# Performance work log

Hardware: AMD Instinct MI355X
Metric: run time of the kernel (lower is better)

Reference implementation:

```python
import jax, jax.numpy as jnp
import numpy as np

NUM_NODES = 100000
EMB = 16
LAT = 8
EDGE_DIM = 32
E = 1600000


def setup_inputs() -> dict:
    key = jax.random.key(0)
    ks = jax.random.split(key, 12)
    s = 0.05
    return {
        "edge_index": jax.random.randint(ks[0], (2, E), 0, NUM_NODES),
        "edge_attr": jax.random.normal(ks[1], (E, EDGE_DIM), dtype=jnp.float32),
        "node_emb": jax.random.normal(ks[2], (NUM_NODES, EMB), dtype=jnp.float32) * s,
        "ew_W1": jax.random.normal(ks[3], (EDGE_DIM, 64), dtype=jnp.float32) * s,
        "ew_b1": jnp.zeros((64,), jnp.float32),
        "ew_W2": jax.random.normal(ks[4], (64, EMB * LAT), dtype=jnp.float32) * s,
        "ew_b2": jnp.zeros((EMB * LAT,), jnp.float32),
        "root_W": jax.random.normal(ks[5], (EMB, LAT), dtype=jnp.float32) * s,
        "conv_b": jnp.zeros((LAT,), jnp.float32),
        "dec_W1": jax.random.normal(ks[6], (2 * LAT, 64), dtype=jnp.float32) * s,
        "dec_b1": jnp.zeros((64,), jnp.float32),
        "dec_W2": jax.random.normal(ks[7], (64, EDGE_DIM), dtype=jnp.float32) * s,
        "dec_b2": jnp.zeros((EDGE_DIM,), jnp.float32),
    }


def reference(edge_index, edge_attr, node_emb, ew_W1, ew_b1, ew_W2, ew_b2,
              root_W, conv_b, dec_W1, dec_b1, dec_W2, dec_b2):
    src, tgt = edge_index[0], edge_index[1]
    # edge MLP -> per-edge weight matrix (E, EMB, LAT)
    h = jax.nn.relu(edge_attr @ ew_W1 + ew_b1)
    theta = (h @ ew_W2 + ew_b2).reshape(-1, EMB, LAT)
    # per-edge matmul on gathered source features
    msg = jnp.einsum('ei,eio->eo', node_emb[src], theta)  # (E, LAT)
    # scatter-mean to targets
    agg = jax.ops.segment_sum(msg, tgt, num_segments=NUM_NODES)
    cnt = jax.ops.segment_sum(jnp.ones((msg.shape[0],), msg.dtype), tgt, num_segments=NUM_NODES)
    agg = agg / jnp.maximum(cnt, 1.0)[:, None]
    # NNConv root weight + bias
    latent = node_emb @ root_W + agg + conv_b  # (N, LAT)
    # decode: gather-concat-MLP on edges
    edge_in = jnp.concatenate([latent[src], latent[tgt]], axis=1)  # (E, 2*LAT)
    out = jax.nn.relu(edge_in @ dec_W1 + dec_b1) @ dec_W2 + dec_b2  # (E, EDGE_DIM)
    return out
```

## Files before the change

kernel.cpp:

```cpp
#include <hip/hip_runtime.h>
#include <hip/hip_bf16.h>

typedef __attribute__((ext_vector_type(8))) short  s16x8;
typedef __attribute__((ext_vector_type(4))) float  f32x4;

constexpr int EMB  = 16;
constexpr int LAT  = 8;
constexpr int EDIM = 32;
constexpr int HID  = 64;

constexpr int BSHIFT = 7;
constexpr int BNODES = 1 << BSHIFT;
constexpr int PCHUNK = 8192;

__device__ __forceinline__ short f2b(float f) {
  __hip_bfloat16 h = __float2bfloat16(f);
  return __builtin_bit_cast(short, h);
}
__device__ __forceinline__ float asf(unsigned int u) { return __builtin_bit_cast(float, u); }
__device__ __forceinline__ unsigned int pk2(float lo, float hi) {
  return ((unsigned int)(unsigned short)f2b(hi) << 16) |
         (unsigned int)(unsigned short)f2b(lo);
}

#define FIXSCALE 1.0995116277760e12f
#define FIXINV   9.094947017729282e-13

__global__ void prep_kernel(const float* __restrict__ W1, const float* __restrict__ W2,
                            const float* __restrict__ b2,
                            const float* __restrict__ dW1, const float* __restrict__ dW2,
                            short* __restrict__ W1c, short* __restrict__ W2p,
                            unsigned int* __restrict__ b2pp,
                            short* __restrict__ dW1c, short* __restrict__ dW2p) {
  int t = blockIdx.x * blockDim.x + threadIdx.x;
  if (t < 64 * 32) { int c = t / 32, k = t % 32; W1c[t] = f2b(W1[k * 64 + c]); }
  if (t < 8192) {
    int ct2 = t >> 10, kt = (t >> 9) & 1, lh = (t >> 7) & 3, r = (t >> 3) & 15, j = t & 7;
    int k = (kt * 2 + (j >> 2)) * 16 + lh * 4 + (j & 3);
    int i = 2 * ct2 + ((r >> 1) & 1);
    int o = 2 * (r >> 2) + (r & 1);
    W2p[t] = f2b(W2[k * 128 + i * 8 + o]);
  }
  if (t < 64) {
    int lh = t >> 4, slot = t & 15;
    int ct2 = slot >> 1, ih = slot & 1;
    int i = 2 * ct2 + ih;
    unsigned int lo = (unsigned short)f2b(b2[i * 8 + 2 * lh]);
    unsigned int hi = (unsigned short)f2b(b2[i * 8 + 2 * lh + 1]);
    b2pp[t] = (hi << 16) | lo;
  }
  if (t < 64 * 16) { int c = t / 16, k = t % 16; dW1c[t] = f2b(dW1[k * 64 + c]); }
  if (t < 2048) {
    int ct2 = t >> 10, kt = (t >> 9) & 1, lh = (t >> 7) & 3, r = (t >> 3) & 15, j = t & 7;
    int k = (kt * 2 + (j >> 2)) * 16 + lh * 4 + (j & 3);
    dW2p[t] = f2b(dW2[k * 32 + ct2 * 16 + r]);
  }
}

__global__ __launch_bounds__(256) void bhist_kernel(const int* __restrict__ ei,
                                                    int* __restrict__ bins,
                                                    int E, int nbuck) {
  __shared__ int h[1024];
  for (int i = threadIdx.x; i < nbuck; i += 256) h[i] = 0;
  __syncthreads();
  for (int e = blockIdx.x * blockDim.x + threadIdx.x; e < E; e += gridDim.x * blockDim.x)
    atomicAdd(&h[ei[E + e] >> BSHIFT], 1);
  __syncthreads();
  for (int i = threadIdx.x; i < nbuck; i += 256)
    if (h[i]) atomicAdd(&bins[i], h[i]);
}

__global__ __launch_bounds__(1024) void bscan_kernel(const int* __restrict__ bins,
                                                     int* __restrict__ bases,
                                                     int* __restrict__ cursor, int nbuck) {
  __shared__ int sh[1024];
  int tid = threadIdx.x;
  int v = (tid < nbuck) ? bins[tid] : 0;
  sh[tid] = v;
  __syncthreads();
  for (int off = 1; off < 1024; off <<= 1) {
    int t = (tid >= off) ? sh[tid - off] : 0;
    __syncthreads();
    sh[tid] += t;
    __syncthreads();
  }
  int ex = sh[tid] - v;
  if (tid < nbuck) { bases[tid] = ex; cursor[tid] = ex; }
  if (tid == 0) bases[nbuck] = sh[1023];
}

__global__ __launch_bounds__(256) void part_kernel(const int* __restrict__ ei,
                                                   int* __restrict__ cursor,
                                                   unsigned int* __restrict__ recs,
                                                   int E, int nbuck) {
  __shared__ int h[1024];
  __shared__ int gcl[1024];
  __shared__ int lr[1024];
  const int tid  = threadIdx.x;
  const int base = blockIdx.x * PCHUNK;

  for (int i = tid; i < nbuck; i += 256) { h[i] = 0; lr[i] = 0; }
  __syncthreads();
  for (int i = tid; i < PCHUNK; i += 256) {
    int e = base + i;
    if (e < E) atomicAdd(&h[ei[E + e] >> BSHIFT], 1);
  }
  __syncthreads();
  for (int i = tid; i < nbuck; i += 256)
    gcl[i] = h[i] ? atomicAdd(&cursor[i], h[i]) : 0;
  __syncthreads();
  for (int i = tid; i < PCHUNK; i += 256) {
    int e = base + i;
    if (e >= E) continue;
    int tgt = ei[E + e];
    int b = tgt >> BSHIFT;
    int p = gcl[b] + atomicAdd(&lr[b], 1);
    recs[p] = ((unsigned int)e << BSHIFT) | (unsigned int)(tgt & (BNODES - 1));
  }
}

__global__ __launch_bounds__(256, 2) void encagg_kernel(
    const int* __restrict__ ei, const float* __restrict__ attr,
    const float* __restrict__ emb,
    const short* __restrict__ W1c, const float* __restrict__ b1,
    const short* __restrict__ W2p, const unsigned int* __restrict__ b2pp,
    const unsigned int* __restrict__ recs, const int* __restrict__ bases,
    const float* __restrict__ rootW, const float* __restrict__ convb,
    float* __restrict__ latent, int N, int E) {
  __shared__ short lds_w1[2048];
  __shared__ short lds_w2[8192];
  __shared__ float lds_b1[64];
  __shared__ unsigned int lds_b2[64];
  __shared__ long long acc[BNODES][LAT];
  __shared__ int cnt[BNODES];
  __shared__ float rw[EMB * LAT];
  __shared__ float cb[LAT];

  const int tid = threadIdx.x;
  const int w = tid >> 6, l = tid & 63;
  const int lh = l >> 4, ll = l & 15;
  const int b = blockIdx.x;

  {
    reinterpret_cast<int4*>(lds_w1)[tid] = reinterpret_cast<const int4*>(W1c)[tid];
#pragma unroll
    for (int i = 0; i < 4; i++)
      reinterpret_cast<int4*>(lds_w2)[i * 256 + tid] =
          reinterpret_cast<const int4*>(W2p)[i * 256 + tid];
    if (tid < 64) lds_b1[tid] = b1[tid];
    if (tid < 64) lds_b2[tid] = b2pp[tid];
    long long* af0 = &acc[0][0];
    for (int i = tid; i < BNODES * LAT; i += 256) af0[i] = 0;
    if (tid < BNODES) cnt[tid] = 0;
    if (tid < EMB * LAT) rw[tid] = rootW[tid];
    if (tid < LAT) cb[tid] = convb[tid];
  }
  __syncthreads();

  const int s = bases[b], epos = bases[b + 1];
  const int nrec = epos - s;
  const f32x4 z = {0.f, 0.f, 0.f, 0.f};

  for (int g = w * 64; g < nrec; g += 256) {
    const int base = s + g;
    int ridx = min(base + l, epos - 1);
    unsigned int rec = recs[ridx];
    int eid = (int)(rec >> BSHIFT);
    int tl  = (int)(rec & (BNODES - 1));
    unsigned int xqp[8];
    {
      int src = ei[eid];
      const float4* er = reinterpret_cast<const float4*>(emb) + (size_t)src * 4;
      float4 v0 = er[0], v1 = er[1], v2 = er[2], v3 = er[3];
      xqp[0] = pk2(v0.x, v0.y); xqp[1] = pk2(v0.z, v0.w);
      xqp[2] = pk2(v1.x, v1.y); xqp[3] = pk2(v1.z, v1.w);
      xqp[4] = pk2(v2.x, v2.y); xqp[5] = pk2(v2.z, v2.w);
      xqp[6] = pk2(v3.x, v3.y); xqp[7] = pk2(v3.z, v3.w);
    }
    s16x8 afs[4];
#pragma unroll
    for (int mt = 0; mt < 4; mt++) {
      int rowE = __shfl(eid, mt * 16 + ll, 64);
      const float4* ap = reinterpret_cast<const float4*>(attr + (size_t)rowE * EDIM + lh * 8);
      float4 a0 = ap[0], a1 = ap[1];
      afs[mt][0]=f2b(a0.x); afs[mt][1]=f2b(a0.y); afs[mt][2]=f2b(a0.z); afs[mt][3]=f2b(a0.w);
      afs[mt][4]=f2b(a1.x); afs[mt][5]=f2b(a1.y); afs[mt][6]=f2b(a1.z); afs[mt][7]=f2b(a1.w);
    }

#pragma unroll
    for (int mt = 0; mt < 4; mt++) {
      f32x4 c1t[4];
#pragma unroll
      for (int ct = 0; ct < 4; ct++) {
        s16x8 b1f = *reinterpret_cast<const s16x8*>(lds_w1 + (ct * 16 + ll) * 32 + lh * 8);
        c1t[ct] = __builtin_amdgcn_mfma_f32_16x16x32_bf16(b1f, afs[mt], z, 0, 0, 0);
      }
      short hb[4][4];
#pragma unroll
      for (int ct = 0; ct < 4; ct++) {
        float4 bv = *reinterpret_cast<const float4*>(lds_b1 + ct * 16 + lh * 4);
        hb[ct][0] = f2b(fmaxf(c1t[ct][0] + bv.x, 0.f));
        hb[ct][1] = f2b(fmaxf(c1t[ct][1] + bv.y, 0.f));
        hb[ct][2] = f2b(fmaxf(c1t[ct][2] + bv.z, 0.f));
        hb[ct][3] = f2b(fmaxf(c1t[ct][3] + bv.w, 0.f));
      }
      s16x8 a2f0, a2f1;
#pragma unroll
      for (int j = 0; j < 8; j++) a2f0[j] = hb[(j >> 2)][j & 3];
#pragma unroll
      for (int j = 0; j < 8; j++) a2f1[j] = hb[2 + (j >> 2)][j & 3];

      const int srcl = mt * 16 + ll;
      unsigned int xs[8];
#pragma unroll
      for (int c = 0; c < 8; c++)
        xs[c] = (unsigned int)__shfl((int)xqp[c], srcl, 64);
      int tlv = __shfl(tl, srcl, 64);

      float q0 = 0.f, q1 = 0.f;
#pragma unroll
      for (int ct2 = 0; ct2 < 8; ct2++) {
        s16x8 f0 = *reinterpret_cast<const s16x8*>(lds_w2 + ((ct2 * 2 + 0) * 4 + lh) * 128 + ll * 8);
        s16x8 f1 = *reinterpret_cast<const s16x8*>(lds_w2 + ((ct2 * 2 + 1) * 4 + lh) * 128 + ll * 8);
        f32x4 c2 = __builtin_amdgcn_mfma_f32_16x16x32_bf16(f0, a2f0, z, 0, 0, 0);
        c2 = __builtin_amdgcn_mfma_f32_16x16x32_bf16(f1, a2f1, c2, 0, 0, 0);
        uint2 pp = *reinterpret_cast<const uint2*>(lds_b2 + lh * 16 + 2 * ct2);
        float b00 = asf(pp.x << 16), b01 = asf(pp.x & 0xffff0000u);
        float b10 = asf(pp.y << 16), b11 = asf(pp.y & 0xffff0000u);
        float xv0 = asf(xs[ct2] << 16);
        float xv1 = asf(xs[ct2] & 0xffff0000u);
        q0 = fmaf(xv0, c2[0] + b00, q0);
        q1 = fmaf(xv0, c2[1] + b01, q1);
        q0 = fmaf(xv1, c2[2] + b10, q0);
        q1 = fmaf(xv1, c2[3] + b11, q1);
      }
      if (base + srcl < epos) {
        atomicAdd((unsigned long long*)&acc[tlv][2 * lh],
                  (unsigned long long)(long long)(q0 * FIXSCALE));
        atomicAdd((unsigned long long*)&acc[tlv][2 * lh + 1],
                  (unsigned long long)(long long)(q1 * FIXSCALE));
        if (lh == 0) atomicAdd(&cnt[tlv], 1);
      }
    }
  }
  __syncthreads();

  int n = b * BNODES + tid;
  if (tid < BNODES && n < N) {
    float inv = 1.f / fmaxf((float)cnt[tid], 1.f);
    float r[LAT];
#pragma unroll
    for (int o = 0; o < LAT; o++)
      r[o] = fmaf((float)((double)acc[tid][o] * FIXINV), inv, cb[o]);

    float x[EMB];
    const float4* np4 = reinterpret_cast<const float4*>(emb) + (size_t)n * (EMB / 4);
#pragma unroll
    for (int i = 0; i < EMB / 4; i++) {
      float4 v = np4[i];
      x[4 * i + 0] = v.x; x[4 * i + 1] = v.y; x[4 * i + 2] = v.z; x[4 * i + 3] = v.w;
    }
#pragma unroll
    for (int i = 0; i < EMB; i++)
#pragma unroll
      for (int o = 0; o < LAT; o++) r[o] = fmaf(x[i], rw[i * LAT + o], r[o]);

    float4* lp = reinterpret_cast<float4*>(latent) + (size_t)n * 2;
    lp[0] = make_float4(r[0], r[1], r[2], r[3]);
    lp[1] = make_float4(r[4], r[5], r[6], r[7]);
  }
}

__global__ __launch_bounds__(256, 4) void dec_mfma_kernel(
    const int* __restrict__ ei, const float* __restrict__ lat,
    const short* __restrict__ dW1c, const float* __restrict__ db1,
    const short* __restrict__ dW2p, const float* __restrict__ db2,
    float* __restrict__ out, int E) {
  __shared__ short lds_w1[2048];
  __shared__ short lds_w2[2048];
  __shared__ float lds_b1[64];
  __shared__ float lds_b2[32];

  const int tid = threadIdx.x;
  const int w = tid >> 6, l = tid & 63;
  const int lh = l >> 4, ll = l & 15;
  const int ebase = blockIdx.x * 256 + w * 64;

  {
    if (tid < 128) {
      int4 v = reinterpret_cast<const int4*>(dW1c)[tid];
      int hid = tid >> 1, kb = (tid & 1) * 8;
      *reinterpret_cast<int4*>(lds_w1 + hid * 32 + kb) = v;
      *reinterpret_cast<int4*>(lds_w1 + hid * 32 + 16 + kb) = make_int4(0, 0, 0, 0);
    }
    reinterpret_cast<int4*>(lds_w2)[tid] = reinterpret_cast<const int4*>(dW2p)[tid];
    if (tid < 64) lds_b1[tid] = db1[tid];
    if (tid < 32) lds_b2[tid] = db2[tid];
  }
  __syncthreads();

  const f32x4 z = {0.f, 0.f, 0.f, 0.f};

#pragma unroll
  for (int mt = 0; mt < 4; mt++) {
    s16x8 af = (s16x8){0, 0, 0, 0, 0, 0, 0, 0};
    if (lh < 2) {
      int rowA = min(ebase + mt * 16 + ll, E - 1);
      int node = ei[(lh == 0 ? 0 : E) + rowA];
      const float4* lp = reinterpret_cast<const float4*>(lat + (size_t)node * LAT);
      float4 p0 = lp[0], p1 = lp[1];
      af[0]=f2b(p0.x); af[1]=f2b(p0.y); af[2]=f2b(p0.z); af[3]=f2b(p0.w);
      af[4]=f2b(p1.x); af[5]=f2b(p1.y); af[6]=f2b(p1.z); af[7]=f2b(p1.w);
    }

    f32x4 c1t[4];
#pragma unroll
    for (int ct = 0; ct < 4; ct++) {
      s16x8 b1f = *reinterpret_cast<const s16x8*>(lds_w1 + (ct * 16 + ll) * 32 + lh * 8);
      c1t[ct] = __builtin_amdgcn_mfma_f32_16x16x32_bf16(b1f, af, z, 0, 0, 0);
    }

    short hb[4][4];
#pragma unroll
    for (int ct = 0; ct < 4; ct++) {
      float4 bv = *reinterpret_cast<const float4*>(lds_b1 + ct * 16 + lh * 4);
      hb[ct][0] = f2b(fmaxf(c1t[ct][0] + bv.x, 0.f));
      hb[ct][1] = f2b(fmaxf(c1t[ct][1] + bv.y, 0.f));
      hb[ct][2] = f2b(fmaxf(c1t[ct][2] + bv.z, 0.f));
      hb[ct][3] = f2b(fmaxf(c1t[ct][3] + bv.w, 0.f));
    }
    s16x8 a2f0, a2f1;
#pragma unroll
    for (int j = 0; j < 8; j++) a2f0[j] = hb[(j >> 2)][j & 3];
#pragma unroll
    for (int j = 0; j < 8; j++) a2f1[j] = hb[2 + (j >> 2)][j & 3];

    int e = ebase + mt * 16 + ll;
#pragma unroll
    for (int ct2 = 0; ct2 < 2; ct2++) {
      s16x8 f0 = *reinterpret_cast<const s16x8*>(lds_w2 + ((ct2 * 2 + 0) * 4 + lh) * 128 + ll * 8);
      s16x8 f1 = *reinterpret_cast<const s16x8*>(lds_w2 + ((ct2 * 2 + 1) * 4 + lh) * 128 + ll * 8);
      f32x4 c2 = __builtin_amdgcn_mfma_f32_16x16x32_bf16(f0, a2f0, z, 0, 0, 0);
      c2 = __builtin_amdgcn_mfma_f32_16x16x32_bf16(f1, a2f1, c2, 0, 0, 0);
      float4 bv = *reinterpret_cast<const float4*>(lds_b2 + ct2 * 16 + lh * 4);
      if (e < E)
        *reinterpret_cast<float4*>(out + (size_t)e * EDIM + ct2 * 16 + lh * 4) =
            make_float4(c2[0] + bv.x, c2[1] + bv.y, c2[2] + bv.z, c2[3] + bv.w);
    }
  }
}

extern "C" void kernel_launch(void* const* d_in, const int* in_sizes, int n_in,
                              void* d_out, int out_size, void* d_ws, size_t ws_size,
                              hipStream_t stream) {
  const int*   ei    = (const int*)  d_in[0];
  const float* attr  = (const float*)d_in[1];
  const float* emb   = (const float*)d_in[2];
  const float* ewW1  = (const float*)d_in[3];
  const float* ewb1  = (const float*)d_in[4];
  const float* ewW2  = (const float*)d_in[5];
  const float* ewb2  = (const float*)d_in[6];
  const float* rootW = (const float*)d_in[7];
  const float* convb = (const float*)d_in[8];
  const float* dW1   = (const float*)d_in[9];
  const float* db1   = (const float*)d_in[10];
  const float* dW2   = (const float*)d_in[11];
  const float* db2   = (const float*)d_in[12];
  float* out = (float*)d_out;

  const int E     = in_sizes[0] / 2;
  const int N     = in_sizes[2] / EMB;
  const int nbuck = (N + BNODES - 1) >> BSHIFT;

  short* W1c  = (short*)d_ws;
  short* W2p  = W1c + 64 * 32;
  short* dW1c = W2p + 8192;
  short* dW2p = dW1c + 64 * 16;
  unsigned int* b2pp = (unsigned int*)(dW2p + 2048);
  float* lat  = (float*)(b2pp + 64);
  unsigned int* recs = (unsigned int*)(lat + (size_t)N * LAT);
  int* bins   = (int*)(recs + E);
  int* bases  = bins + nbuck;
  int* cursor = bases + nbuck + 1;

  const int blocks_e = (E + 255) / 256;
  const int blocks_p = (E + PCHUNK - 1) / PCHUNK;

  hipMemsetAsync(bins, 0, (size_t)nbuck * sizeof(int), stream);
  prep_kernel<<<32, 256, 0, stream>>>(ewW1, ewW2, ewb2, dW1, dW2,
                                      W1c, W2p, b2pp, dW1c, dW2p);
  bhist_kernel<<<256, 256, 0, stream>>>(ei, bins, E, nbuck);
  bscan_kernel<<<1, 1024, 0, stream>>>(bins, bases, cursor, nbuck);
  part_kernel<<<blocks_p, 256, 0, stream>>>(ei, cursor, recs, E, nbuck);
  encagg_kernel<<<nbuck, 256, 0, stream>>>(ei, attr, emb, W1c, ewb1, W2p, b2pp,
                                           recs, bases, rootW, convb, lat, N, E);
  dec_mfma_kernel<<<blocks_e, 256, 0, stream>>>(ei, lat, dW1c, db1, dW2p, db2, out, E);
}
```

Baseline: 223.2 us.

## Halve node buckets, pre-swizzle MFMA weight fragments, pad accumulator, raise occupancy

Node buckets shrink from 128 to 64 nodes, which doubles the number of encode/aggregate blocks, and the scan now handles two bins per thread to cover up to 2048 buckets. First-layer weights for the encoder and decoder are pre-swizzled into a fragment-contiguous layout so each lane's LDS read is contiguous, replacing the strided reads. The shared int64 accumulator gets a padding column to cut bank conflicts, and the encoder launch bound moves to 4 blocks per CU. In exchange, each block does less work relative to its fixed cost of loading weights into LDS, and the extra blocks and higher occupancy put more pressure on registers.

```diff
diff --git a/kernel.cpp b/kernel.cpp
--- a/kernel.cpp
+++ b/kernel.cpp
@@ -9,9 +9,10 @@
 constexpr int EDIM = 32;
 constexpr int HID  = 64;
 
-constexpr int BSHIFT = 7;
+constexpr int BSHIFT = 6;
 constexpr int BNODES = 1 << BSHIFT;
 constexpr int PCHUNK = 8192;
+constexpr int MAXBUCK = 2048;
 
 __device__ __forceinline__ short f2b(float f) {
   __hip_bfloat16 h = __float2bfloat16(f);
@@ -29,11 +30,14 @@
 __global__ void prep_kernel(const float* __restrict__ W1, const float* __restrict__ W2,
                             const float* __restrict__ b2,
                             const float* __restrict__ dW1, const float* __restrict__ dW2,
-                            short* __restrict__ W1c, short* __restrict__ W2p,
+                            short* __restrict__ W1f, short* __restrict__ W2p,
                             unsigned int* __restrict__ b2pp,
-                            short* __restrict__ dW1c, short* __restrict__ dW2p) {
+                            short* __restrict__ dW1f, short* __restrict__ dW2p) {
   int t = blockIdx.x * blockDim.x + threadIdx.x;
-  if (t < 64 * 32) { int c = t / 32, k = t % 32; W1c[t] = f2b(W1[k * 64 + c]); }
+  if (t < 2048) {
+    int j = t & 7, ll = (t >> 3) & 15, lh = (t >> 7) & 3, ct = t >> 9;
+    W1f[t] = f2b(W1[(lh * 8 + j) * 64 + ct * 16 + ll]);
+  }
   if (t < 8192) {
     int ct2 = t >> 10, kt = (t >> 9) & 1, lh = (t >> 7) & 3, r = (t >> 3) & 15, j = t & 7;
     int k = (kt * 2 + (j >> 2)) * 16 + lh * 4 + (j & 3);
@@ -49,7 +53,10 @@
     unsigned int hi = (unsigned short)f2b(b2[i * 8 + 2 * lh + 1]);
     b2pp[t] = (hi << 16) | lo;
   }
-  if (t < 64 * 16) { int c = t / 16, k = t % 16; dW1c[t] = f2b(dW1[k * 64 + c]); }
+  if (t < 4096) {
+    int j = t & 7, ll = (t >> 3) & 15, lh = (t >> 7) & 3, ct = t >> 9;
+    dW1f[t] = (lh < 2) ? f2b(dW1[(lh * 8 + j) * 64 + ct * 16 + ll]) : (short)0;
+  }
   if (t < 2048) {
     int ct2 = t >> 10, kt = (t >> 9) & 1, lh = (t >> 7) & 3, r = (t >> 3) & 15, j = t & 7;
     int k = (kt * 2 + (j >> 2)) * 16 + lh * 4 + (j & 3);
@@ -60,7 +67,7 @@
 __global__ __launch_bounds__(256) void bhist_kernel(const int* __restrict__ ei,
                                                     int* __restrict__ bins,
                                                     int E, int nbuck) {
-  __shared__ int h[1024];
+  __shared__ int h[MAXBUCK];
   for (int i = threadIdx.x; i < nbuck; i += 256) h[i] = 0;
   __syncthreads();
   for (int e = blockIdx.x * blockDim.x + threadIdx.x; e < E; e += gridDim.x * blockDim.x)
@@ -75,8 +82,10 @@
                                                      int* __restrict__ cursor, int nbuck) {
   __shared__ int sh[1024];
   int tid = threadIdx.x;
-  int v = (tid < nbuck) ? bins[tid] : 0;
-  sh[tid] = v;
+  int v0 = (2 * tid     < nbuck) ? bins[2 * tid]     : 0;
+  int v1 = (2 * tid + 1 < nbuck) ? bins[2 * tid + 1] : 0;
+  int s = v0 + v1;
+  sh[tid] = s;
   __syncthreads();
   for (int off = 1; off < 1024; off <<= 1) {
     int t = (tid >= off) ? sh[tid - off] : 0;
@@ -84,8 +93,9 @@
     sh[tid] += t;
     __syncthreads();
   }
-  int ex = sh[tid] - v;
-  if (tid < nbuck) { bases[tid] = ex; cursor[tid] = ex; }
+  int ex = sh[tid] - s;
+  if (2 * tid < nbuck)     { bases[2 * tid] = ex;          cursor[2 * tid] = ex; }
+  if (2 * tid + 1 < nbuck) { bases[2 * tid + 1] = ex + v0; cursor[2 * tid + 1] = ex + v0; }
   if (tid == 0) bases[nbuck] = sh[1023];
 }
 
@@ -93,9 +103,9 @@
                                                    int* __restrict__ cursor,
                                                    unsigned int* __restrict__ recs,
                                                    int E, int nbuck) {
-  __shared__ int h[1024];
-  __shared__ int gcl[1024];
-  __shared__ int lr[1024];
+  __shared__ int h[MAXBUCK];
+  __shared__ int gcl[MAXBUCK];
+  __shared__ int lr[MAXBUCK];
   const int tid  = threadIdx.x;
   const int base = blockIdx.x * PCHUNK;
 
@@ -119,10 +129,10 @@
   }
 }
 
-__global__ __launch_bounds__(256, 2) void encagg_kernel(
+__global__ __launch_bounds__(256, 4) void encagg_kernel(
     const int* __restrict__ ei, const float* __restrict__ attr,
     const float* __restrict__ emb,
-    const short* __restrict__ W1c, const float* __restrict__ b1,
+    const short* __restrict__ W1f, const float* __restrict__ b1,
     const short* __restrict__ W2p, const unsigned int* __restrict__ b2pp,
     const unsigned int* __restrict__ recs, const int* __restrict__ bases,
     const float* __restrict__ rootW, const float* __restrict__ convb,
@@ -131,7 +141,7 @@
   __shared__ short lds_w2[8192];
   __shared__ float lds_b1[64];
   __shared__ unsigned int lds_b2[64];
-  __shared__ long long acc[BNODES][LAT];
+  __shared__ long long acc[BNODES][LAT + 1];
   __shared__ int cnt[BNODES];
   __shared__ float rw[EMB * LAT];
   __shared__ float cb[LAT];
@@ -142,7 +152,7 @@
   const int b = blockIdx.x;
 
   {
-    reinterpret_cast<int4*>(lds_w1)[tid] = reinterpret_cast<const int4*>(W1c)[tid];
+    reinterpret_cast<int4*>(lds_w1)[tid] = reinterpret_cast<const int4*>(W1f)[tid];
 #pragma unroll
     for (int i = 0; i < 4; i++)
       reinterpret_cast<int4*>(lds_w2)[i * 256 + tid] =
@@ -150,7 +160,7 @@
     if (tid < 64) lds_b1[tid] = b1[tid];
     if (tid < 64) lds_b2[tid] = b2pp[tid];
     long long* af0 = &acc[0][0];
-    for (int i = tid; i < BNODES * LAT; i += 256) af0[i] = 0;
+    for (int i = tid; i < BNODES * (LAT + 1); i += 256) af0[i] = 0;
     if (tid < BNODES) cnt[tid] = 0;
     if (tid < EMB * LAT) rw[tid] = rootW[tid];
     if (tid < LAT) cb[tid] = convb[tid];
@@ -192,7 +202,7 @@
       f32x4 c1t[4];
 #pragma unroll
       for (int ct = 0; ct < 4; ct++) {
-        s16x8 b1f = *reinterpret_cast<const s16x8*>(lds_w1 + (ct * 16 + ll) * 32 + lh * 8);
+        s16x8 b1f = *reinterpret_cast<const s16x8*>(lds_w1 + ((ct * 4 + lh) * 16 + ll) * 8);
         c1t[ct] = __builtin_amdgcn_mfma_f32_16x16x32_bf16(b1f, afs[mt], z, 0, 0, 0);
       }
       short hb[4][4];
@@ -273,10 +283,10 @@
 
 __global__ __launch_bounds__(256, 4) void dec_mfma_kernel(
     const int* __restrict__ ei, const float* __restrict__ lat,
-    const short* __restrict__ dW1c, const float* __restrict__ db1,
+    const short* __restrict__ dW1f, const float* __restrict__ db1,
     const short* __restrict__ dW2p, const float* __restrict__ db2,
     float* __restrict__ out, int E) {
-  __shared__ short lds_w1[2048];
+  __shared__ short lds_w1[4096];
   __shared__ short lds_w2[2048];
   __shared__ float lds_b1[64];
   __shared__ float lds_b2[32];
@@ -287,12 +297,10 @@
   const int ebase = blockIdx.x * 256 + w * 64;
 
   {
-    if (tid < 128) {
-      int4 v = reinterpret_cast<const int4*>(dW1c)[tid];
-      int hid = tid >> 1, kb = (tid & 1) * 8;
-      *reinterpret_cast<int4*>(lds_w1 + hid * 32 + kb) = v;
-      *reinterpret_cast<int4*>(lds_w1 + hid * 32 + 16 + kb) = make_int4(0, 0, 0, 0);
-    }
+#pragma unroll
+    for (int i = 0; i < 2; i++)
+      reinterpret_cast<int4*>(lds_w1)[i * 256 + tid] =
+          reinterpret_cast<const int4*>(dW1f)[i * 256 + tid];
     reinterpret_cast<int4*>(lds_w2)[tid] = reinterpret_cast<const int4*>(dW2p)[tid];
     if (tid < 64) lds_b1[tid] = db1[tid];
     if (tid < 32) lds_b2[tid] = db2[tid];
@@ -316,7 +324,7 @@
     f32x4 c1t[4];
 #pragma unroll
     for (int ct = 0; ct < 4; ct++) {
-      s16x8 b1f = *reinterpret_cast<const s16x8*>(lds_w1 + (ct * 16 + ll) * 32 + lh * 8);
+      s16x8 b1f = *reinterpret_cast<const s16x8*>(lds_w1 + ((ct * 4 + lh) * 16 + ll) * 8);
       c1t[ct] = __builtin_amdgcn_mfma_f32_16x16x32_bf16(b1f, af, z, 0, 0, 0);
     }
 
@@ -372,10 +380,10 @@
   const int N     = in_sizes[2] / EMB;
   const int nbuck = (N + BNODES - 1) >> BSHIFT;
 
-  short* W1c  = (short*)d_ws;
-  short* W2p  = W1c + 64 * 32;
-  short* dW1c = W2p + 8192;
-  short* dW2p = dW1c + 64 * 16;
+  short* W1f  = (short*)d_ws;
+  short* W2p  = W1f + 2048;
+  short* dW1f = W2p + 8192;
+  short* dW2p = dW1f + 4096;
   unsigned int* b2pp = (unsigned int*)(dW2p + 2048);
   float* lat  = (float*)(b2pp + 64);
   unsigned int* recs = (unsigned int*)(lat + (size_t)N * LAT);
@@ -388,11 +396,11 @@
 
   hipMemsetAsync(bins, 0, (size_t)nbuck * sizeof(int), stream);
   prep_kernel<<<32, 256, 0, stream>>>(ewW1, ewW2, ewb2, dW1, dW2,
-                                      W1c, W2p, b2pp, dW1c, dW2p);
+                                      W1f, W2p, b2pp, dW1f, dW2p);
   bhist_kernel<<<256, 256, 0, stream>>>(ei, bins, E, nbuck);
   bscan_kernel<<<1, 1024, 0, stream>>>(bins, bases, cursor, nbuck);
   part_kernel<<<blocks_p, 256, 0, stream>>>(ei, cursor, recs, E, nbuck);
-  encagg_kernel<<<nbuck, 256, 0, stream>>>(ei, attr, emb, W1c, ewb1, W2p, b2pp,
+  encagg_kernel<<<nbuck, 256, 0, stream>>>(ei, attr, emb, W1f, ewb1, W2p, b2pp,
                                            recs, bases, rootW, convb, lat, N, E);
-  dec_mfma_kernel<<<blocks_e, 256, 0, stream>>>(ei, lat, dW1c, db1, dW2p, db2, out, E);
-}
+  dec_mfma_kernel<<<blocks_e, 256, 0, stream>>>(ei, lat, dW1f, db1, dW2p, db2, out, E);
+}
```

Result: slower. 516.6 us (+131.4%).
